# Performance work log

Hardware: AMD Instinct MI355X
Metric: run time of the kernel (lower is better)

The kernel has to match this reference:

```python
import jax, jax.numpy as jnp
import numpy as np

N = 4096
NHID = 256
K1, K2, K3 = 3072, 2304, 1728


def _layernorm(x, g, b, eps=1e-5):
    m = jnp.mean(x, axis=-1, keepdims=True)
    v = jnp.mean((x - m) ** 2, axis=-1, keepdims=True)
    return (x - m) / jnp.sqrt(v + eps) * g + b


def _gcn(x, A, W, b):
    # PyG GCNConv: add self loops, symmetric norm D^-1/2 (A+I) D^-1/2,
    # messages flow row(source) -> col(target): out[j] = sum_i Anorm[i,j] (xW)[i] + b
    n = A.shape[0]
    A_sl = A + jnp.eye(n, dtype=A.dtype)
    deg = A_sl.sum(0)  # in-degree over col index incl. self loop
    dinv = jnp.where(deg > 0, deg ** -0.5, 0.0)
    An = A_sl * dinv[:, None] * dinv[None, :]
    return An.T @ (x @ W) + b


def _sagpool(x, A, Wp, bp, k):
    score = jnp.tanh(_gcn(x, A, Wp, bp)[:, 0])  # [n]
    vals, perm = jax.lax.top_k(score, k)
    x_new = x[perm] * vals[:, None]
    A_new = A[perm][:, perm]  # induced subgraph of directed edges
    return x_new, A_new


def _readout(x):
    # cat([global_max_pool, global_mean_pool]) for a single graph -> [1, 2*nhid]
    return jnp.concatenate([x.max(0), x.mean(0)])[None, :]


def setup_inputs() -> dict:
    key = jax.random.key(0)
    ks = jax.random.split(key, 10)
    s = 0.05
    return {
        'feature': jax.random.normal(ks[0], (N, 500), jnp.float32),
        'img_info': jax.random.normal(ks[1], (N, 6), jnp.float32),
        'Wp': jax.random.normal(ks[2], (6, 12), jnp.float32) * s,
        'bp': jnp.zeros((12,), jnp.float32),
        'ln_f_g': jnp.ones((500,), jnp.float32),
        'ln_f_b': jnp.zeros((500,), jnp.float32),
        'ln_p_g': jnp.ones((12,), jnp.float32),
        'ln_p_b': jnp.zeros((12,), jnp.float32),
        'W1': jax.random.normal(ks[3], (512, NHID), jnp.float32) * s,
        'b1': jnp.zeros((NHID,), jnp.float32),
        'Wpool1': jax.random.normal(ks[4], (NHID, 1), jnp.float32) * s,
        'bpool1': jnp.zeros((1,), jnp.float32),
        'W2': jax.random.normal(ks[5], (NHID, NHID), jnp.float32) * s,
        'b2': jnp.zeros((NHID,), jnp.float32),
        'Wpool2': jax.random.normal(ks[6], (NHID, 1), jnp.float32) * s,
        'bpool2': jnp.zeros((1,), jnp.float32),
        'W3': jax.random.normal(ks[7], (NHID, NHID), jnp.float32) * s,
        'b3': jnp.zeros((NHID,), jnp.float32),
        'Wpool3': jax.random.normal(ks[8], (NHID, 1), jnp.float32) * s,
        'bpool3': jnp.zeros((1,), jnp.float32),
    }


def reference(feature, img_info, Wp, bp, ln_f_g, ln_f_b, ln_p_g, ln_p_b,
              W1, b1, Wpool1, bpool1, W2, b2, Wpool2, bpool2,
              W3, b3, Wpool3, bpool3):
    # pos embedding + self-attention over nodes
    pos = img_info @ Wp + bp                                  # [N,12]
    att = jax.nn.softmax(pos @ pos.T / jnp.sqrt(12.0), axis=1)  # [N,N]
    pos = att @ pos

    f = _layernorm(feature, ln_f_g, ln_f_b)
    p = _layernorm(pos, ln_p_g, ln_p_b)
    x0 = jnp.concatenate([f, p], axis=1)                      # [N,512]

    # edge construction: upper-triangular directed edges where sqdist < 0.5*max sqdist
    sq = jnp.sum(x0 * x0, axis=1)
    d2 = sq[:, None] - 2.0 * (x0 @ x0.T) + sq[None, :]        # [N,N]
    t = 0.5 * d2.max()
    n = x0.shape[0]
    iu = jnp.triu(jnp.ones((n, n), bool), 1)
    A = jnp.where((d2 < t) & iu, 1.0, 0.0).astype(x0.dtype)

    x = jax.nn.relu(_gcn(x0, A, W1, b1))
    x, A = _sagpool(x, A, Wpool1, bpool1, K1)
    x1 = _readout(x)

    x = jax.nn.relu(_gcn(x, A, W2, b2))
    x, A = _sagpool(x, A, Wpool2, bpool2, K2)
    x2 = _readout(x)

    x = jax.nn.relu(_gcn(x, A, W3, b3))
    x, A = _sagpool(x, A, Wpool3, bpool3, K3)
    x3 = _readout(x)

    return x1 + x2 + x3  # [1, 512]
```

## Files before the change

kernel.cpp:

```cpp
#include <hip/hip_runtime.h>
#include <math.h>

#define NN 4096
#define RB 128

typedef __attribute__((ext_vector_type(8))) short bf16x8;
typedef __attribute__((ext_vector_type(4))) float f32x4;

__device__ __forceinline__ unsigned encf(float f) {
  unsigned u = __float_as_uint(f);
  return (u & 0x80000000u) ? ~u : (u | 0x80000000u);
}
__device__ __forceinline__ float decf(unsigned u) {
  return __uint_as_float((u & 0x80000000u) ? (u ^ 0x80000000u) : ~u);
}
__device__ __forceinline__ unsigned short f2bf(float f) {
  unsigned u = __float_as_uint(f);
  return (unsigned short)((u + 0x7fffu + ((u >> 16) & 1u)) >> 16);
}

__global__ void k_pos(const float* img, const float* Wp, const float* bp, float* pos,
                      unsigned* dmax) {
  if (blockIdx.x == 0 && threadIdx.x == 0) *dmax = 0u;
  int t = blockIdx.x * 256 + threadIdx.x;
  if (t >= NN * 12) return;
  int i = t / 12, d = t % 12;
  float s = bp[d];
#pragma unroll
  for (int k = 0; k < 6; ++k) s += img[i * 6 + k] * Wp[k * 12 + d];
  pos[t] = s;
}

__global__ __launch_bounds__(256) void k_attn3(const float* pos, float* out) {
  __shared__ float sp[12][256];
  int t = threadIdx.x, lane = t & 63, w = t >> 6;
  int ib = blockIdx.x * 8 + w * 2;
  float pi[2][12];
#pragma unroll
  for (int r = 0; r < 2; ++r)
#pragma unroll
    for (int d = 0; d < 12; ++d) pi[r][d] = pos[(ib + r) * 12 + d] * 0.28867513459481287f;
  float sl[2] = {0.f, 0.f};
  float acc[2][12] = {};
  const float4* p4 = (const float4*)pos;
  for (int kt = 0; kt < NN; kt += 256) {
    __syncthreads();
    int j = kt + t;
    float4 a = p4[j * 3 + 0], b = p4[j * 3 + 1], c = p4[j * 3 + 2];
    sp[0][t] = a.x; sp[1][t] = a.y; sp[2][t] = a.z; sp[3][t] = a.w;
    sp[4][t] = b.x; sp[5][t] = b.y; sp[6][t] = b.z; sp[7][t] = b.w;
    sp[8][t] = c.x; sp[9][t] = c.y; sp[10][t] = c.z; sp[11][t] = c.w;
    __syncthreads();
#pragma unroll
    for (int q = 0; q < 4; ++q) {
      int jj = q * 64 + lane;
      float pj[12];
#pragma unroll
      for (int d = 0; d < 12; ++d) pj[d] = sp[d][jj];
#pragma unroll
      for (int r = 0; r < 2; ++r) {
        float s = 0.f;
#pragma unroll
        for (int d = 0; d < 12; ++d) s = fmaf(pi[r][d], pj[d], s);
        float e = __expf(s);
        sl[r] += e;
#pragma unroll
        for (int d = 0; d < 12; ++d) acc[r][d] = fmaf(e, pj[d], acc[r][d]);
      }
    }
  }
#pragma unroll
  for (int r = 0; r < 2; ++r) {
    float s = sl[r];
#pragma unroll
    for (int o = 32; o > 0; o >>= 1) s += __shfl_xor(s, o);
    float ad[12];
#pragma unroll
    for (int d = 0; d < 12; ++d) {
      ad[d] = acc[r][d];
#pragma unroll
      for (int o = 32; o > 0; o >>= 1) ad[d] += __shfl_xor(ad[d], o);
    }
    if (lane == 0) {
      float inv = 1.f / s;
#pragma unroll
      for (int d = 0; d < 12; ++d) out[(ib + r) * 12 + d] = ad[d] * inv;
    }
  }
}

__global__ __launch_bounds__(256) void k_lnx(const float* f, const float* g, const float* b,
                                             const float* p, const float* pg, const float* pb,
                                             float* x0, unsigned short* x0h, float* sqv,
                                             int* degA) {
  __shared__ float row[512];
  __shared__ float wrA[4], wrB[4], wrC[4];
  int i = blockIdx.x, t = threadIdx.x, lane = t & 63, w = t >> 6;
  if (t == 0) degA[i] = 0;
  float v1 = f[i * 500 + t];
  float v2 = (t < 244) ? f[i * 500 + 256 + t] : 0.f;
  float part = v1 + v2;
#pragma unroll
  for (int o = 32; o > 0; o >>= 1) part += __shfl_xor(part, o);
  if (lane == 0) wrA[w] = part;
  __syncthreads();
  float m = (wrA[0] + wrA[1] + wrA[2] + wrA[3]) * (1.f / 500.f);
  float d1 = v1 - m, d2 = v2 - m;
  float pvv = d1 * d1 + ((t < 244) ? d2 * d2 : 0.f);
#pragma unroll
  for (int o = 32; o > 0; o >>= 1) pvv += __shfl_xor(pvv, o);
  if (lane == 0) wrB[w] = pvv;
  __syncthreads();
  float scale = 1.f / sqrtf((wrB[0] + wrB[1] + wrB[2] + wrB[3]) * (1.f / 500.f) + 1e-5f);
  row[t] = d1 * scale * g[t] + b[t];
  if (t < 244) row[256 + t] = d2 * scale * g[256 + t] + b[256 + t];
  if (t >= 244) {
    int tt = t - 244;
    float pv[12], pm = 0.f;
#pragma unroll
    for (int d = 0; d < 12; ++d) { pv[d] = p[i * 12 + d]; pm += pv[d]; }
    pm *= (1.f / 12.f);
    float pvar = 0.f;
#pragma unroll
    for (int d = 0; d < 12; ++d) { float dd = pv[d] - pm; pvar += dd * dd; }
    pvar *= (1.f / 12.f);
    float ps = 1.f / sqrtf(pvar + 1e-5f);
    row[500 + tt] = (pv[tt] - pm) * ps * pg[tt] + pb[tt];
  }
  __syncthreads();
  float a = row[t], c = row[256 + t];
  float sq = a * a + c * c;
#pragma unroll
  for (int o = 32; o > 0; o >>= 1) sq += __shfl_xor(sq, o);
  if (lane == 0) wrC[w] = sq;
  __syncthreads();
  if (t == 0) sqv[i] = wrC[0] + wrC[1] + wrC[2] + wrC[3];
  x0[(size_t)i * 512 + t] = a;
  x0[(size_t)i * 512 + 256 + t] = c;
  x0h[(size_t)i * 512 + t] = f2bf(a);
  x0h[(size_t)i * 512 + 256 + t] = f2bf(c);
}

#define BK 64
template <bool MASK>
__global__ __launch_bounds__(256) void k_d2m(const unsigned short* X, const float* sqv,
                                             unsigned* dmax, float* tileMin,
                                             unsigned char* ATm, int* deg) {
  __shared__ unsigned short As[2][128 * BK];
  __shared__ unsigned short Bs[2][128 * BK];
  __shared__ float wmax[4], wmin[4];
  const int NT = NN / 128;
  int bid0 = blockIdx.x;
  int bid = (bid0 & 7) * 66 + (bid0 >> 3);
  int ti = 0, rem = bid;
  while (rem >= NT - ti) { rem -= NT - ti; ++ti; }
  int tj = ti + rem;
  int t = threadIdx.x, lane = t & 63, w = t >> 6;
  int wr = w >> 1, wc = w & 1;
  const unsigned short* Abase = X + (size_t)ti * 128 * 512;
  const unsigned short* Bbase = X + (size_t)tj * 128 * 512;
  int lr = lane >> 3, lc = lane & 7;

  float thr = 0.f;
  if (MASK) {
    thr = 0.5f * decf(*dmax);
    uint4 z = make_uint4(0u, 0u, 0u, 0u);
    if (ti != tj) {
#pragma unroll
      for (int q0 = 0; q0 < 4; ++q0) {
        int q = t + q0 * 256; int r = q >> 3, c4 = q & 7;
        *(uint4*)(ATm + (size_t)(ti * 128 + r) * NN + tj * 128 + c4 * 16) = z;
      }
    }
    if (tileMin[blockIdx.x] >= thr) {
#pragma unroll
      for (int q0 = 0; q0 < 4; ++q0) {
        int q = t + q0 * 256; int r = q >> 3, c4 = q & 7;
        *(uint4*)(ATm + (size_t)(tj * 128 + r) * NN + ti * 128 + c4 * 16) = z;
      }
      return;
    }
  }

  auto stage = [&](int buf, int k0) {
#pragma unroll
    for (int i = 0; i < 4; ++i) {
      int q = w * 4 + i;
      int r = q * 8 + lr;
      int cs = lc ^ (r & 7);
      __builtin_amdgcn_global_load_lds(
          (const __attribute__((address_space(1))) unsigned int*)(Abase + (size_t)r * 512 + k0 + cs * 8),
          (__attribute__((address_space(3))) unsigned int*)(&As[buf][q * 512]), 16, 0, 0);
      __builtin_amdgcn_global_load_lds(
          (const __attribute__((address_space(1))) unsigned int*)(Bbase + (size_t)r * 512 + k0 + cs * 8),
          (__attribute__((address_space(3))) unsigned int*)(&Bs[buf][q * 512]), 16, 0, 0);
    }
  };

  stage(0, 0);

  f32x4 acc[4][4] = {};
  int rl = lane & 15, kg = lane >> 4;
  for (int step = 0; step < 8; ++step) {
    int cur = step & 1;
    if (step < 7) {
      stage(cur ^ 1, (step + 1) * BK);
      asm volatile("s_waitcnt vmcnt(8)" ::: "memory");
    } else {
      asm volatile("s_waitcnt vmcnt(0)" ::: "memory");
    }
    __builtin_amdgcn_sched_barrier(0);
    __builtin_amdgcn_s_barrier();
    __builtin_amdgcn_s_setprio(1);
#pragma unroll
    for (int ks = 0; ks < 2; ++ks) {
      bf16x8 af[4], bq[4];
#pragma unroll
      for (int f = 0; f < 4; ++f) {
        int rA = wr * 64 + f * 16 + rl;
        af[f] = *(const bf16x8*)(&As[cur][rA * BK + (((ks * 4 + kg) ^ (rA & 7)) << 3)]);
        int rB = wc * 64 + f * 16 + rl;
        bq[f] = *(const bf16x8*)(&Bs[cur][rB * BK + (((ks * 4 + kg) ^ (rB & 7)) << 3)]);
      }
#pragma unroll
      for (int a = 0; a < 4; ++a)
#pragma unroll
        for (int b = 0; b < 4; ++b)
          acc[a][b] = __builtin_amdgcn_mfma_f32_16x16x32_bf16(af[a], bq[b], acc[a][b], 0, 0, 0);
    }
    __builtin_amdgcn_s_setprio(0);
    __builtin_amdgcn_sched_barrier(0);
    __builtin_amdgcn_s_barrier();
  }
  int rbase = ti * 128 + wr * 64 + ((lane >> 4) << 2);
  int cbase = tj * 128 + wc * 64 + (lane & 15);
  if (!MASK) {
    float lm = -1e30f, lmin = 1e30f;
#pragma unroll
    for (int a = 0; a < 4; ++a) {
      float si[4];
#pragma unroll
      for (int r = 0; r < 4; ++r) si[r] = sqv[rbase + a * 16 + r];
#pragma unroll
      for (int b = 0; b < 4; ++b) {
        int gj = cbase + b * 16;
        float sj = sqv[gj];
#pragma unroll
        for (int r = 0; r < 4; ++r) {
          float d2v = si[r] - 2.f * acc[a][b][r] + sj;
          lm = fmaxf(lm, d2v);
          if (rbase + a * 16 + r < gj) lmin = fminf(lmin, d2v);
        }
      }
    }
#pragma unroll
    for (int o = 32; o > 0; o >>= 1) {
      lm = fmaxf(lm, __shfl_xor(lm, o));
      lmin = fminf(lmin, __shfl_xor(lmin, o));
    }
    if (lane == 0) { wmax[w] = lm; wmin[w] = lmin; }
    __syncthreads();
    if (t == 0) {
      atomicMax(dmax, encf(fmaxf(fmaxf(wmax[0], wmax[1]), fmaxf(wmax[2], wmax[3]))));
      tileMin[blockIdx.x] = fminf(fminf(wmin[0], wmin[1]), fminf(wmin[2], wmin[3]));
    }
  } else {
#pragma unroll
    for (int b = 0; b < 4; ++b) {
      int gj = cbase + b * 16;
      float sj = sqv[gj];
      int rowcnt = 0;
#pragma unroll
      for (int a = 0; a < 4; ++a) {
        int gi0 = rbase + a * 16;
        union { unsigned char c[4]; unsigned u; } m4;
#pragma unroll
        for (int r = 0; r < 4; ++r) {
          float d2v = sqv[gi0 + r] - 2.f * acc[a][b][r] + sj;
          unsigned char mv = (d2v < thr && (gi0 + r) < gj) ? 1 : 0;
          m4.c[r] = mv; rowcnt += mv;
        }
        *(unsigned*)(ATm + (size_t)gj * NN + gi0) = m4.u;
      }
      if (rowcnt) atomicAdd(&deg[gj], rowcnt);
    }
  }
}

__global__ __launch_bounds__(256) void k_gemm(const float* A, const float* B, const int* deg,
                                              float* C, int M, int N, int K) {
  __shared__ float Ast[16][34];
  __shared__ float Bs[16][64];
  int t = threadIdx.x, tx = t & 15, ty = t >> 4;
  int nbx = N >> 6;
  int total = gridDim.x;
  int bid0 = blockIdx.x;
  int bid = (bid0 & 7) * (total >> 3) + (bid0 >> 3);
  int m0 = (bid / nbx) * 32, n0 = (bid % nbx) * 64;
  int ar = t >> 3, ac = (t * 2) & 15;
  int br = t >> 4, bc = (t & 15) * 4;
  float2 ra = *(const float2*)(A + (size_t)(m0 + ar) * K + ac);
  float4 rb = *(const float4*)(B + (size_t)br * N + n0 + bc);
  float acc[2][4] = {};
  for (int k0 = 0; k0 < K; k0 += 16) {
    Ast[ac][ar] = ra.x; Ast[ac + 1][ar] = ra.y;
    *(float4*)(&Bs[br][bc]) = rb;
    __syncthreads();
    if (k0 + 16 < K) {
      ra = *(const float2*)(A + (size_t)(m0 + ar) * K + k0 + 16 + ac);
      rb = *(const float4*)(B + (size_t)(k0 + 16 + br) * N + n0 + bc);
    }
#pragma unroll
    for (int kk = 0; kk < 16; ++kk) {
      float2 av = *(const float2*)(&Ast[kk][ty * 2]);
      float4 bv = *(const float4*)(&Bs[kk][tx * 4]);
      acc[0][0] = fmaf(av.x, bv.x, acc[0][0]);
      acc[0][1] = fmaf(av.x, bv.y, acc[0][1]);
      acc[0][2] = fmaf(av.x, bv.z, acc[0][2]);
      acc[0][3] = fmaf(av.x, bv.w, acc[0][3]);
      acc[1][0] = fmaf(av.y, bv.x, acc[1][0]);
      acc[1][1] = fmaf(av.y, bv.y, acc[1][1]);
      acc[1][2] = fmaf(av.y, bv.z, acc[1][2]);
      acc[1][3] = fmaf(av.y, bv.w, acc[1][3]);
    }
    __syncthreads();
  }
#pragma unroll
  for (int a = 0; a < 2; ++a) {
    float dv = 1.f / sqrtf((float)(1 + deg[m0 + ty * 2 + a]));
#pragma unroll
    for (int b2 = 0; b2 < 4; ++b2)
      C[(size_t)(m0 + ty * 2 + a) * N + n0 + tx * 4 + b2] = acc[a][b2] * dv;
  }
}

__global__ __launch_bounds__(256) void k_agg(const float* y, const unsigned char* ATm,
                                             const int* deg, const float* bias,
                                             const float* Wpool, const float* bp,
                                             float* out, float* y2, float* score, int n) {
  __shared__ unsigned char mrow[256];
  __shared__ int s_any;
  __shared__ float wred[4];
  int j = blockIdx.x, t = threadIdx.x, lane = t & 63, w = t >> 6;
  int dg = deg[j];
  float dj = 1.f / sqrtf((float)(1 + dg));
  float acc = y[(size_t)j * 256 + t];
  if (dg != 0) {
    for (int i0 = 0; i0 < n; i0 += 256) {
      if (t == 0) s_any = 0;
      __syncthreads();
      unsigned char m = ATm[(size_t)j * n + i0 + t];
      mrow[t] = m;
      if (m) s_any = 1;
      __syncthreads();
      if (s_any) {
        for (int u = 0; u < 256; ++u)
          if (mrow[u]) acc += y[(size_t)(i0 + u) * 256 + t];
      }
      __syncthreads();
    }
  }
  float o = fmaxf(dj * acc + bias[t], 0.f);
  out[(size_t)j * 256 + t] = o;
  float rv = o * Wpool[t];
#pragma unroll
  for (int os = 32; os > 0; os >>= 1) rv += __shfl_xor(rv, os);
  if (lane == 0) wred[w] = rv;
  __syncthreads();
  if (t == 0) {
    float yy = dj * (wred[0] + wred[1] + wred[2] + wred[3]);
    y2[j] = yy;
    if (dg == 0) score[j] = tanhf(dj * yy + bp[0]);
  }
}

__global__ __launch_bounds__(256) void k_scorek(const float* y2, const unsigned char* ATm,
                                                const int* deg, const float* bp,
                                                float* score, int n) {
  int w = threadIdx.x >> 6, lane = threadIdx.x & 63;
  int j = blockIdx.x * 4 + w;
  if (j >= n) return;
  int dg = deg[j];
  if (dg == 0) return;
  float dj = 1.f / sqrtf((float)(1 + dg));
  float s = 0.f;
  const uint4* row = (const uint4*)(ATm + (size_t)j * n);
  for (int p = lane; p < n / 16; p += 64) {
    uint4 v = row[p];
    if (v.x | v.y | v.z | v.w) {
      int base = p * 16;
#pragma unroll
      for (int q = 0; q < 4; ++q) {
        unsigned u = (&v.x)[q];
#pragma unroll
        for (int b2 = 0; b2 < 4; ++b2)
          if ((u >> (8 * b2)) & 0xffu) s += y2[base + q * 4 + b2];
      }
    }
  }
  for (int sh = 32; sh > 0; sh >>= 1) s += __shfl_down(s, sh);
  if (lane == 0) score[j] = tanhf(dj * (y2[j] + s) + bp[0]);
}

__global__ __launch_bounds__(1024) void k_topsel(const float* score, int n, int k,
                                                 int* perm, float* vals) {
  __shared__ unsigned keys[4096];
  __shared__ unsigned hist[256];
  __shared__ unsigned s_state[2];
  __shared__ unsigned woff[16];
  int t = threadIdx.x, lane = t & 63, w = t >> 6;
  for (int i = t; i < 4096; i += 1024) keys[i] = (i < n) ? encf(score[i]) : 0u;
  if (t == 0) { s_state[0] = 0u; s_state[1] = (unsigned)k; }
  __syncthreads();

  for (int pass = 0; pass < 4; ++pass) {
    int shift = 24 - pass * 8;
    if (t < 256) hist[t] = 0u;
    __syncthreads();
    unsigned prefix = s_state[0];
    unsigned need = s_state[1];
    unsigned pmask = pass ? (0xFFFFFFFFu << (shift + 8)) : 0u;
    for (int i = t; i < n; i += 1024) {
      unsigned kk = keys[i];
      if ((kk & pmask) == prefix) atomicAdd(&hist[(kk >> shift) & 255u], 1u);
    }
    __syncthreads();
    if (w == 0) {
      unsigned h[4], suf[4];
#pragma unroll
      for (int r = 0; r < 4; ++r) h[r] = hist[lane * 4 + r];
      suf[3] = h[3]; suf[2] = h[2] + suf[3]; suf[1] = h[1] + suf[2]; suf[0] = h[0] + suf[1];
      unsigned lsum = suf[0];
      unsigned s = lsum;
#pragma unroll
      for (int off = 1; off < 64; off <<= 1) {
        unsigned o = __shfl_down(s, off);
        if (lane + off < 64) s += o;
      }
      unsigned Hl = s - lsum;
      int cand = -1; unsigned cumAt = 0, histAt = 0;
#pragma unroll
      for (int r = 0; r < 4; ++r) {
        unsigned c = Hl + suf[r];
        if (c >= need) { cand = lane * 4 + r; cumAt = c; histAt = h[r]; }
      }
      int gmax = cand;
#pragma unroll
      for (int off = 32; off > 0; off >>= 1) {
        int o = __shfl_xor(gmax, off);
        gmax = o > gmax ? o : gmax;
      }
      if (cand == gmax && cand >= 0) {
        s_state[0] = prefix | ((unsigned)cand << shift);
        s_state[1] = need - (cumAt - histAt);
      }
    }
    __syncthreads();
  }
  unsigned cutoff = s_state[0];
  unsigned tcount = s_state[1];
  unsigned G = (unsigned)k - tcount;

  int i0 = t * 4;
  unsigned loc[4], cnt = 0;
#pragma unroll
  for (int r = 0; r < 4; ++r) {
    unsigned kk = keys[i0 + r];
    unsigned g = (kk > cutoff) ? 1u : 0u;
    unsigned e = (kk == cutoff) ? 1u : 0u;
    loc[r] = cnt;
    cnt += (g << 16) | e;
  }
  unsigned inc = cnt;
#pragma unroll
  for (int off = 1; off < 64; off <<= 1) {
    unsigned o = __shfl_up(inc, off);
    if (lane >= off) inc += o;
  }
  if (lane == 63) woff[w] = inc;
  __syncthreads();
  if (t == 0) {
    unsigned run = 0;
    for (int q = 0; q < 16; ++q) { unsigned v = woff[q]; woff[q] = run; run += v; }
  }
  __syncthreads();
  unsigned base = woff[w] + (inc - cnt);
#pragma unroll
  for (int r = 0; r < 4; ++r) {
    unsigned kk = keys[i0 + r];
    unsigned p = base + loc[r];
    if (kk > cutoff) {
      unsigned pos = p >> 16;
      perm[pos] = i0 + r; vals[pos] = decf(kk);
    } else if (kk == cutoff) {
      unsigned pe = p & 0xffffu;
      if (pe < tcount) { perm[G + pe] = i0 + r; vals[G + pe] = decf(kk); }
    }
  }
}

__global__ __launch_bounds__(256) void k_pool(const float* xg, const int* perm, const float* vals,
                                              float* xp, float* pmax, float* psum, int k,
                                              const unsigned char* ATold, const int* degCur,
                                              unsigned char* ATnew, int* degNext, int nold) {
  __shared__ int sperm[4096];
  __shared__ int redi[256];
  int b = blockIdx.x, t = threadIdx.x;
  if (b < RB) {
    float m = -1e30f, s = 0.f;
    for (int r = b; r < k; r += RB) {
      float v = xg[(size_t)perm[r] * 256 + t] * vals[r];
      if (xp) xp[(size_t)r * 256 + t] = v;
      m = fmaxf(m, v); s += v;
    }
    pmax[b * 256 + t] = m; psum[b * 256 + t] = s;
    return;
  }
  int c = b - RB;
  int src = perm[c];
  if (degCur[src] == 0) {
    if (t == 0) degNext[c] = 0;
    return;
  }
  for (int r = t; r < k; r += 256) sperm[r] = perm[r];
  __syncthreads();
  unsigned char* orow = ATnew + (size_t)c * k;
  const unsigned char* row = ATold + (size_t)src * nold;
  int cnt = 0;
  for (int r = t; r < k; r += 256) { unsigned char v = row[sperm[r]]; orow[r] = v; cnt += v; }
  redi[t] = cnt; __syncthreads();
  for (int s = 128; s > 0; s >>= 1) { if (t < s) redi[t] += redi[t + s]; __syncthreads(); }
  if (t == 0) degNext[c] = redi[0];
}

__global__ void k_rfin3(const float* pm0, const float* ps0, int k0,
                        const float* pm1, const float* ps1, int k1,
                        const float* pm2, const float* ps2, int k2, float* out) {
  int t = threadIdx.x;
  float m0 = -1e30f, s0 = 0.f, m1 = -1e30f, s1 = 0.f, m2 = -1e30f, s2 = 0.f;
  for (int q = 0; q < RB; ++q) {
    m0 = fmaxf(m0, pm0[q * 256 + t]); s0 += ps0[q * 256 + t];
    m1 = fmaxf(m1, pm1[q * 256 + t]); s1 += ps1[q * 256 + t];
    m2 = fmaxf(m2, pm2[q * 256 + t]); s2 += ps2[q * 256 + t];
  }
  out[t] = m0 + m1 + m2;
  out[256 + t] = s0 / (float)k0 + s1 / (float)k1 + s2 / (float)k2;
}

static void run_layer(hipStream_t stream, const float* x_in, int n, int inC,
                      const float* W, const float* b, const float* Wpool, const float* bpool,
                      int k, const unsigned char* ATcur, unsigned char* ATnext,
                      const int* degCur, int* degNext,
                      float* ybuf, float* xg, float* xp, float* y2,
                      float* score, int* perm, float* vals, float* pmax, float* psum) {
  k_gemm<<<(n / 32) * 4, 256, 0, stream>>>(x_in, W, degCur, ybuf, n, 256, inC);
  k_agg<<<n, 256, 0, stream>>>(ybuf, ATcur, degCur, b, Wpool, bpool, xg, y2, score, n);
  k_scorek<<<n / 4, 256, 0, stream>>>(y2, ATcur, degCur, bpool, score, n);
  k_topsel<<<1, 1024, 0, stream>>>(score, n, k, perm, vals);
  int grid = RB + (ATnext ? k : 0);
  k_pool<<<grid, 256, 0, stream>>>(xg, perm, vals, ATnext ? xp : nullptr, pmax, psum, k,
                                   ATcur, degCur, ATnext, degNext, n);
}

extern "C" void kernel_launch(void* const* d_in, const int* in_sizes, int n_in,
                              void* d_out, int out_size, void* d_ws, size_t ws_size,
                              hipStream_t stream) {
  const float* feature = (const float*)d_in[0];
  const float* img     = (const float*)d_in[1];
  const float* Wp      = (const float*)d_in[2];
  const float* bp      = (const float*)d_in[3];
  const float* ln_f_g  = (const float*)d_in[4];
  const float* ln_f_b  = (const float*)d_in[5];
  const float* ln_p_g  = (const float*)d_in[6];
  const float* ln_p_b  = (const float*)d_in[7];
  const float* W1 = (const float*)d_in[8];   const float* b1 = (const float*)d_in[9];
  const float* Wpool1 = (const float*)d_in[10]; const float* bpool1 = (const float*)d_in[11];
  const float* W2 = (const float*)d_in[12];  const float* b2 = (const float*)d_in[13];
  const float* Wpool2 = (const float*)d_in[14]; const float* bpool2 = (const float*)d_in[15];
  const float* W3 = (const float*)d_in[16];  const float* b3 = (const float*)d_in[17];
  const float* Wpool3 = (const float*)d_in[18]; const float* bpool3 = (const float*)d_in[19];
  float* out = (float*)d_out;
  (void)in_sizes; (void)n_in; (void)out_size; (void)ws_size;

  char* w = (char*)d_ws;
  size_t off = 0;
  auto alloc = [&](size_t bytes) -> char* {
    off = (off + 255) & ~(size_t)255;
    char* p = w + off;
    off += bytes;
    return p;
  };
  float* pos0 = (float*)alloc((size_t)NN * 12 * 4);
  float* pos1 = (float*)alloc((size_t)NN * 12 * 4);
  float* x0   = (float*)alloc((size_t)NN * 512 * 4);
  unsigned short* x0h = (unsigned short*)alloc((size_t)NN * 512 * 2);
  float* sqv  = (float*)alloc((size_t)NN * 4);
  unsigned* dmax = (unsigned*)alloc(4);
  float* tileMin = (float*)alloc(528 * 4);
  int* degA = (int*)alloc((size_t)NN * 4);
  int* degB = (int*)alloc((size_t)NN * 4);
  float* ybuf = (float*)alloc((size_t)NN * 256 * 4);
  float* xg   = (float*)alloc((size_t)NN * 256 * 4);
  float* xp   = (float*)alloc((size_t)NN * 256 * 4);
  float* y2   = (float*)alloc((size_t)NN * 4);
  float* score= (float*)alloc((size_t)NN * 4);
  int*   perm = (int*)alloc((size_t)NN * 4);
  float* vals = (float*)alloc((size_t)NN * 4);
  float* pmax0 = (float*)alloc(RB * 256 * 4);
  float* psum0 = (float*)alloc(RB * 256 * 4);
  float* pmax1 = (float*)alloc(RB * 256 * 4);
  float* psum1 = (float*)alloc(RB * 256 * 4);
  float* pmax2 = (float*)alloc(RB * 256 * 4);
  float* psum2 = (float*)alloc(RB * 256 * 4);
  unsigned char* ATa = (unsigned char*)alloc((size_t)NN * NN);
  unsigned char* ATb = (unsigned char*)alloc((size_t)3072 * 3072);

  k_pos<<<(NN * 12 + 255) / 256, 256, 0, stream>>>(img, Wp, bp, pos0, dmax);
  k_attn3<<<NN / 8, 256, 0, stream>>>(pos0, pos1);
  k_lnx<<<NN, 256, 0, stream>>>(feature, ln_f_g, ln_f_b, pos1, ln_p_g, ln_p_b,
                                x0, x0h, sqv, degA);

  const int NT = NN / 128, TT = NT * (NT + 1) / 2;
  k_d2m<false><<<TT, 256, 0, stream>>>(x0h, sqv, dmax, tileMin, nullptr, nullptr);
  k_d2m<true><<<TT, 256, 0, stream>>>(x0h, sqv, dmax, tileMin, ATa, degA);

  run_layer(stream, x0, 4096, 512, W1, b1, Wpool1, bpool1, 3072, ATa, ATb, degA, degB,
            ybuf, xg, xp, y2, score, perm, vals, pmax0, psum0);
  run_layer(stream, xp, 3072, 256, W2, b2, Wpool2, bpool2, 2304, ATb, ATa, degB, degA,
            ybuf, xg, xp, y2, score, perm, vals, pmax1, psum1);
  run_layer(stream, xp, 2304, 256, W3, b3, Wpool3, bpool3, 1728, ATa, nullptr, degA, nullptr,
            ybuf, xg, xp, y2, score, perm, vals, pmax2, psum2);
  k_rfin3<<<1, 256, 0, stream>>>(pmax0, psum0, 3072, pmax1, psum1, 2304,
                                 pmax2, psum2, 1728, out);
}
```

Baseline: 215.3 us.

## Fuse pos projection into attention kernel and skip zeroing of all-empty row blocks

Removes the separate k_pos kernel by recomputing the 6x12 position projection inside the attention kernel, for both query rows and streamed key tiles, and moves the dmax reset into k_lnx. Adds a per-row-block minimum distance (rowMin), tracked with atomicMin in the first d2m pass. The masking pass uses it to skip zero-filling adjacency tiles whose row block can never contain an edge, cutting redundant writes to the 16MB mask. The trade is extra recomputed FMAs in attention and a dependence on later consumers never reading those unwritten regions.

```diff
diff --git a/kernel.cpp b/kernel.cpp
--- a/kernel.cpp
+++ b/kernel.cpp
@@ -19,37 +19,45 @@
   return (unsigned short)((u + 0x7fffu + ((u >> 16) & 1u)) >> 16);
 }
 
-__global__ void k_pos(const float* img, const float* Wp, const float* bp, float* pos,
-                      unsigned* dmax) {
-  if (blockIdx.x == 0 && threadIdx.x == 0) *dmax = 0u;
-  int t = blockIdx.x * 256 + threadIdx.x;
-  if (t >= NN * 12) return;
-  int i = t / 12, d = t % 12;
-  float s = bp[d];
-#pragma unroll
-  for (int k = 0; k < 6; ++k) s += img[i * 6 + k] * Wp[k * 12 + d];
-  pos[t] = s;
-}
-
-__global__ __launch_bounds__(256) void k_attn3(const float* pos, float* out) {
+__global__ __launch_bounds__(256) void k_attn3(const float* img, const float* Wp,
+                                               const float* bp, float* out) {
   __shared__ float sp[12][256];
+  __shared__ float wp[72];
+  __shared__ float bpd[12];
   int t = threadIdx.x, lane = t & 63, w = t >> 6;
   int ib = blockIdx.x * 8 + w * 2;
+  if (t < 72) wp[t] = Wp[t];
+  if (t < 12) bpd[t] = bp[t];
+  __syncthreads();
   float pi[2][12];
 #pragma unroll
-  for (int r = 0; r < 2; ++r)
-#pragma unroll
-    for (int d = 0; d < 12; ++d) pi[r][d] = pos[(ib + r) * 12 + d] * 0.28867513459481287f;
+  for (int r = 0; r < 2; ++r) {
+    float iv[6];
+#pragma unroll
+    for (int k = 0; k < 6; ++k) iv[k] = img[(ib + r) * 6 + k];
+#pragma unroll
+    for (int d = 0; d < 12; ++d) {
+      float s = bpd[d];
+#pragma unroll
+      for (int k = 0; k < 6; ++k) s += iv[k] * wp[k * 12 + d];
+      pi[r][d] = s * 0.28867513459481287f;
+    }
+  }
   float sl[2] = {0.f, 0.f};
   float acc[2][12] = {};
-  const float4* p4 = (const float4*)pos;
   for (int kt = 0; kt < NN; kt += 256) {
     __syncthreads();
     int j = kt + t;
-    float4 a = p4[j * 3 + 0], b = p4[j * 3 + 1], c = p4[j * 3 + 2];
-    sp[0][t] = a.x; sp[1][t] = a.y; sp[2][t] = a.z; sp[3][t] = a.w;
-    sp[4][t] = b.x; sp[5][t] = b.y; sp[6][t] = b.z; sp[7][t] = b.w;
-    sp[8][t] = c.x; sp[9][t] = c.y; sp[10][t] = c.z; sp[11][t] = c.w;
+    float iv[6];
+#pragma unroll
+    for (int k = 0; k < 6; ++k) iv[k] = img[j * 6 + k];
+#pragma unroll
+    for (int d = 0; d < 12; ++d) {
+      float s = bpd[d];
+#pragma unroll
+      for (int k = 0; k < 6; ++k) s += iv[k] * wp[k * 12 + d];
+      sp[d][t] = s;
+    }
     __syncthreads();
 #pragma unroll
     for (int q = 0; q < 4; ++q) {
@@ -92,11 +100,15 @@
 __global__ __launch_bounds__(256) void k_lnx(const float* f, const float* g, const float* b,
                                              const float* p, const float* pg, const float* pb,
                                              float* x0, unsigned short* x0h, float* sqv,
-                                             int* degA) {
+                                             int* degA, unsigned* dmax, unsigned* rowMin) {
   __shared__ float row[512];
   __shared__ float wrA[4], wrB[4], wrC[4];
   int i = blockIdx.x, t = threadIdx.x, lane = t & 63, w = t >> 6;
   if (t == 0) degA[i] = 0;
+  if (i == 0) {
+    if (t == 0) *dmax = 0u;
+    if (t < 32) rowMin[t] = 0xFFFFFFFFu;
+  }
   float v1 = f[i * 500 + t];
   float v2 = (t < 244) ? f[i * 500 + 256 + t] : 0.f;
   float part = v1 + v2;
@@ -144,7 +156,7 @@
 #define BK 64
 template <bool MASK>
 __global__ __launch_bounds__(256) void k_d2m(const unsigned short* X, const float* sqv,
-                                             unsigned* dmax, float* tileMin,
+                                             unsigned* dmax, float* tileMin, unsigned* rowMin,
                                              unsigned char* ATm, int* deg) {
   __shared__ unsigned short As[2][128 * BK];
   __shared__ unsigned short Bs[2][128 * BK];
@@ -164,8 +176,9 @@
   float thr = 0.f;
   if (MASK) {
     thr = 0.5f * decf(*dmax);
+    unsigned eth = encf(thr);
     uint4 z = make_uint4(0u, 0u, 0u, 0u);
-    if (ti != tj) {
+    if (ti != tj && rowMin[ti] < eth) {
 #pragma unroll
       for (int q0 = 0; q0 < 4; ++q0) {
         int q = t + q0 * 256; int r = q >> 3, c4 = q & 7;
@@ -173,10 +186,12 @@
       }
     }
     if (tileMin[blockIdx.x] >= thr) {
-#pragma unroll
-      for (int q0 = 0; q0 < 4; ++q0) {
-        int q = t + q0 * 256; int r = q >> 3, c4 = q & 7;
-        *(uint4*)(ATm + (size_t)(tj * 128 + r) * NN + ti * 128 + c4 * 16) = z;
+      if (rowMin[tj] < eth) {
+#pragma unroll
+        for (int q0 = 0; q0 < 4; ++q0) {
+          int q = t + q0 * 256; int r = q >> 3, c4 = q & 7;
+          *(uint4*)(ATm + (size_t)(tj * 128 + r) * NN + ti * 128 + c4 * 16) = z;
+        }
       }
       return;
     }
@@ -262,7 +277,9 @@
     __syncthreads();
     if (t == 0) {
       atomicMax(dmax, encf(fmaxf(fmaxf(wmax[0], wmax[1]), fmaxf(wmax[2], wmax[3]))));
-      tileMin[blockIdx.x] = fminf(fminf(wmin[0], wmin[1]), fminf(wmin[2], wmin[3]));
+      float tmin = fminf(fminf(wmin[0], wmin[1]), fminf(wmin[2], wmin[3]));
+      tileMin[blockIdx.x] = tmin;
+      atomicMin(&rowMin[tj], encf(tmin));
     }
   } else {
 #pragma unroll
@@ -590,13 +607,13 @@
     off += bytes;
     return p;
   };
-  float* pos0 = (float*)alloc((size_t)NN * 12 * 4);
   float* pos1 = (float*)alloc((size_t)NN * 12 * 4);
   float* x0   = (float*)alloc((size_t)NN * 512 * 4);
   unsigned short* x0h = (unsigned short*)alloc((size_t)NN * 512 * 2);
   float* sqv  = (float*)alloc((size_t)NN * 4);
   unsigned* dmax = (unsigned*)alloc(4);
   float* tileMin = (float*)alloc(528 * 4);
+  unsigned* rowMin = (unsigned*)alloc(32 * 4);
   int* degA = (int*)alloc((size_t)NN * 4);
   int* degB = (int*)alloc((size_t)NN * 4);
   float* ybuf = (float*)alloc((size_t)NN * 256 * 4);
@@ -615,14 +632,13 @@
   unsigned char* ATa = (unsigned char*)alloc((size_t)NN * NN);
   unsigned char* ATb = (unsigned char*)alloc((size_t)3072 * 3072);
 
-  k_pos<<<(NN * 12 + 255) / 256, 256, 0, stream>>>(img, Wp, bp, pos0, dmax);
-  k_attn3<<<NN / 8, 256, 0, stream>>>(pos0, pos1);
+  k_attn3<<<NN / 8, 256, 0, stream>>>(img, Wp, bp, pos1);
   k_lnx<<<NN, 256, 0, stream>>>(feature, ln_f_g, ln_f_b, pos1, ln_p_g, ln_p_b,
-                                x0, x0h, sqv, degA);
+                                x0, x0h, sqv, degA, dmax, rowMin);
 
   const int NT = NN / 128, TT = NT * (NT + 1) / 2;
-  k_d2m<false><<<TT, 256, 0, stream>>>(x0h, sqv, dmax, tileMin, nullptr, nullptr);
-  k_d2m<true><<<TT, 256, 0, stream>>>(x0h, sqv, dmax, tileMin, ATa, degA);
+  k_d2m<false><<<TT, 256, 0, stream>>>(x0h, sqv, dmax, tileMin, rowMin, nullptr, nullptr);
+  k_d2m<true><<<TT, 256, 0, stream>>>(x0h, sqv, dmax, tileMin, rowMin, ATa, degA);
 
   run_layer(stream, x0, 4096, 512, W1, b1, Wpool1, bpool1, 3072, ATa, ATb, degA, degB,
             ybuf, xg, xp, y2, score, perm, vals, pmax0, psum0);
```

New measurement: 214.5 us. No clear change (-0.4%).
